# Kernel tuning notes

Measured on AMD Instinct MI355X. Metric: run time of the kernel, lower is better.

Reference implementation:

```python
import jax, jax.numpy as jnp
import numpy as np

B, C, L, OUT = 64, 256, 4096, 256
EPS = 1e-5


def setup_inputs() -> dict:
    key = jax.random.key(0)
    ks = jax.random.split(key, 8)
    s = 1.0 / np.sqrt(C)
    return {
        "x": jax.random.normal(ks[0], (B, C, L), dtype=jnp.float32),
        "Wq": jax.random.normal(ks[1], (C, C), dtype=jnp.float32) * s,
        "Wk": jax.random.normal(ks[2], (C, C), dtype=jnp.float32) * s,
        "Wv": jax.random.normal(ks[3], (C, C), dtype=jnp.float32) * s,
        "Wc": jax.random.normal(ks[4], (C, C), dtype=jnp.float32) * s,
        "Wout": jax.random.normal(ks[5], (OUT, C), dtype=jnp.float32) * s,
        "gamma": jnp.ones((C,), dtype=jnp.float32),
        "beta": jnp.zeros((C,), dtype=jnp.float32),
    }


def _conv1x1(W, x):
    # 1x1 Conv1d, no bias: (O,C) x (B,C,L) -> (B,O,L)
    return jnp.einsum("oc,bcl->bol", W, x)


def reference(x, Wq, Wk, Wv, Wc, Wout, gamma, beta):
    q = _conv1x1(Wq, x)  # (B,C,L)
    k = _conv1x1(Wk, x)  # (B,C,L)
    v = _conv1x1(Wv, x)  # (B,C,L)
    # batch-wise attention: att[b,d,l] = sum_c q[b,c,l]*k[d,c,l] / sqrt(C)
    att = jnp.einsum("bcl,dcl->bdl", q, k) / jnp.sqrt(jnp.asarray(C, x.dtype))
    att = jax.nn.softmax(att, axis=1)  # softmax over the key-batch axis
    # virt[b,c,l] = sum_d att[b,d,l] * v[d,c,l]
    virt = jnp.einsum("bdl,dcl->bcl", att, v)
    # GroupNorm(1, C): normalize over (C,L) per sample, per-channel affine
    mean = jnp.mean(virt, axis=(1, 2), keepdims=True)
    var = jnp.var(virt, axis=(1, 2), keepdims=True)
    virt = (virt - mean) * jax.lax.rsqrt(var + EPS)
    virt = virt * gamma[None, :, None] + beta[None, :, None]
    virt = jax.nn.relu(virt)
    virt = _conv1x1(Wc, virt)
    # dropout is identity in eval mode
    y = x + virt
    return _conv1x1(Wout, y)
```

## Files before the change

### kernel.cpp

```cpp
#include <hip/hip_runtime.h>


typedef __attribute__((ext_vector_type(8))) short          v8s;
typedef __attribute__((ext_vector_type(8))) unsigned short v8u;
typedef __attribute__((ext_vector_type(4))) unsigned short v4u;
typedef __attribute__((ext_vector_type(4))) float          f32x4;

#define MFMA16(a, b, c) __builtin_amdgcn_mfma_f32_16x16x32_bf16((a), (b), (c), 0, 0, 0)

static __device__ __forceinline__ unsigned short f2bf(float f) {
  union { float f; unsigned u; } v; v.f = f;
  unsigned r = (v.u + 0x7FFFu + ((v.u >> 16) & 1u)) >> 16;
  return (unsigned short)r;
}
static __device__ __forceinline__ float bf2f(unsigned short h) {
  union { unsigned u; float f; } v; v.u = ((unsigned)h) << 16; return v.f;
}

__global__ void k_prep(const float* __restrict__ Wq, const float* __restrict__ Wk,
                       const float* __restrict__ Wv, const float* __restrict__ Wc,
                       const float* __restrict__ Wout,
                       unsigned short* __restrict__ Wtv,
                       unsigned short* __restrict__ Wout2,
                       float* __restrict__ stats) {
  int bid = blockIdx.x, j = threadIdx.x;
  if (bid < 256) {
    int i = bid;
    float acc = 0.f;
    for (int c = 0; c < 256; ++c) acc += Wq[c * 256 + i] * Wk[c * 256 + j];
    Wtv[i * 256 + j] = f2bf(acc * 0.0625f);
    Wtv[(256 + i) * 256 + j] = f2bf(Wv[i * 256 + j]);
  } else if (bid < 512) {
    int o = bid - 256;
    float acc = 0.f;
    for (int c = 0; c < 256; ++c) acc += Wout[o * 256 + c] * Wc[c * 256 + j];
    Wout2[o * 512 + 256 + j] = f2bf(acc);
    Wout2[o * 512 + j] = f2bf(Wout[o * 256 + j]);
  } else {
    stats[(bid - 512) * 256 + j] = 0.f;
  }
}

__global__ void k_transpose(const float* __restrict__ x, unsigned short* __restrict__ Xt) {
  __shared__ float tile[64 * 65];
  int bid = blockIdx.x;
  int b = bid >> 8, cb = (bid >> 6) & 3, lb = bid & 63;
  int c0 = cb * 64, l0 = lb * 64, t = threadIdx.x;
#pragma unroll
  for (int i = 0; i < 4; ++i) {
    int idx = i * 256 + t, r = idx >> 4, ch = idx & 15;
    float4 v = *(const float4*)(x + ((size_t)(b * 256 + c0 + r)) * 4096 + l0 + ch * 4);
    tile[r * 65 + ch * 4 + 0] = v.x; tile[r * 65 + ch * 4 + 1] = v.y;
    tile[r * 65 + ch * 4 + 2] = v.z; tile[r * 65 + ch * 4 + 3] = v.w;
  }
  __syncthreads();
#pragma unroll
  for (int i = 0; i < 2; ++i) {
    int idx = i * 256 + t, r = idx >> 3, ch = idx & 7;
    v8u o;
#pragma unroll
    for (int j = 0; j < 8; ++j) o[j] = f2bf(tile[(ch * 8 + j) * 65 + r]);
    *(v8u*)(Xt + ((size_t)(b * 4096 + l0 + r)) * 256 + c0 + ch * 8) = o;
  }
}

__global__ __launch_bounds__(512, 4) void k_fused(const unsigned short* __restrict__ Xt,
                                                  const unsigned short* __restrict__ Wtv,
                                                  unsigned short* __restrict__ Virt,
                                                  float* __restrict__ stats) {
  extern __shared__ char smem[];
  unsigned short* Xs  = (unsigned short*)(smem);
  unsigned short* Tb  = (unsigned short*)(smem + 33792);
  unsigned short* Ps  = (unsigned short*)(smem + 70656);
  float*          red = (float*)(smem + 79872);
  float*          rowv= (float*)(smem + 80896);

  int l = blockIdx.x, t = threadIdx.x, lane = t & 63, w = t >> 6;
  int fr = lane & 15, kq = (lane >> 4) * 8, qr = (lane >> 4) * 4;

#pragma unroll
  for (int i = 0; i < 4; ++i) {
    int idx = i * 512 + t, r = idx >> 5, ch = idx & 31;
    *(v8u*)(Xs + r * 264 + ch * 8) = *(const v8u*)(Xt + ((size_t)(r * 4096 + l)) * 256 + ch * 8);
  }
  __syncthreads();

  {
    int n0 = w * 32;
    f32x4 acc[4][2];
#pragma unroll
    for (int mi = 0; mi < 4; ++mi)
#pragma unroll
      for (int nj = 0; nj < 2; ++nj) acc[mi][nj] = (f32x4){0.f, 0.f, 0.f, 0.f};
#pragma unroll
    for (int kc = 0; kc < 8; ++kc) {
      v8s a[4], b[2];
#pragma unroll
      for (int mi = 0; mi < 4; ++mi) a[mi] = *(const v8s*)(Xs + (mi * 16 + fr) * 264 + kc * 32 + kq);
#pragma unroll
      for (int nj = 0; nj < 2; ++nj)
        b[nj] = *(const v8s*)(Wtv + ((size_t)(n0 + nj * 16 + fr)) * 256 + kc * 32 + kq);
#pragma unroll
      for (int mi = 0; mi < 4; ++mi)
#pragma unroll
        for (int nj = 0; nj < 2; ++nj) acc[mi][nj] = MFMA16(a[mi], b[nj], acc[mi][nj]);
    }
#pragma unroll
    for (int mi = 0; mi < 4; ++mi)
#pragma unroll
      for (int nj = 0; nj < 2; ++nj)
#pragma unroll
        for (int i = 0; i < 4; ++i)
          Tb[(mi * 16 + qr + i) * 264 + n0 + nj * 16 + fr] = f2bf(acc[mi][nj][i]);
  }
  __syncthreads();

  int b0 = (w & 3) * 16, dp = (w >> 2) * 2, half = w >> 2;
  f32x4 sacc[2];
  sacc[0] = (f32x4){0.f, 0.f, 0.f, 0.f};
  sacc[1] = (f32x4){0.f, 0.f, 0.f, 0.f};
  {
#pragma unroll
    for (int kc = 0; kc < 8; ++kc) {
      v8s bb = *(const v8s*)(Xs + (b0 + fr) * 264 + kc * 32 + kq);
#pragma unroll
      for (int j = 0; j < 2; ++j) {
        v8s a = *(const v8s*)(Tb + ((dp + j) * 16 + fr) * 264 + kc * 32 + kq);
        sacc[j] = MFMA16(a, bb, sacc[j]);
      }
    }
    float pm = -1e30f;
#pragma unroll
    for (int j = 0; j < 2; ++j)
#pragma unroll
      for (int i = 0; i < 4; ++i) pm = fmaxf(pm, sacc[j][i]);
    pm = fmaxf(pm, __shfl_xor(pm, 16));
    pm = fmaxf(pm, __shfl_xor(pm, 32));
    if (lane < 16) red[(b0 + lane) * 4 + half] = pm;
  }
  __syncthreads();

  {
    float m = fmaxf(red[(b0 + fr) * 4 + 0], red[(b0 + fr) * 4 + 1]);
    float ps = 0.f;
#pragma unroll
    for (int j = 0; j < 2; ++j) {
      v4u pk;
#pragma unroll
      for (int i = 0; i < 4; ++i) {
        float e = __expf(sacc[j][i] - m);
        ps += e;
        pk[i] = f2bf(e);
      }
      *(v4u*)(Ps + (b0 + fr) * 72 + (dp + j) * 16 + qr) = pk;
    }
    ps += __shfl_xor(ps, 16);
    ps += __shfl_xor(ps, 32);
    if (lane < 16) red[(b0 + lane) * 4 + 2 + half] = ps;
  }

  {
    int c0 = w * 32;
    f32x4 vacc[2][4];
#pragma unroll
    for (int ci = 0; ci < 2; ++ci)
#pragma unroll
      for (int di = 0; di < 4; ++di) vacc[ci][di] = (f32x4){0.f, 0.f, 0.f, 0.f};
#pragma unroll
    for (int kc = 0; kc < 8; ++kc) {
      v8s a[2], b[4];
#pragma unroll
      for (int ci = 0; ci < 2; ++ci)
        a[ci] = *(const v8s*)(Wtv + ((size_t)(256 + c0 + ci * 16 + fr)) * 256 + kc * 32 + kq);
#pragma unroll
      for (int di = 0; di < 4; ++di) b[di] = *(const v8s*)(Xs + (di * 16 + fr) * 264 + kc * 32 + kq);
#pragma unroll
      for (int ci = 0; ci < 2; ++ci)
#pragma unroll
        for (int di = 0; di < 4; ++di) vacc[ci][di] = MFMA16(a[ci], b[di], vacc[ci][di]);
    }
#pragma unroll
    for (int ci = 0; ci < 2; ++ci)
#pragma unroll
      for (int di = 0; di < 4; ++di)
#pragma unroll
        for (int i = 0; i < 4; ++i)
          Tb[(c0 + ci * 16 + qr + i) * 72 + di * 16 + fr] = f2bf(vacc[ci][di][i]);
  }
  __syncthreads();

  if (t < 64) rowv[t] = 1.f / (red[t * 4 + 2] + red[t * 4 + 3]);

  f32x4 pacc[4][2];
#pragma unroll
  for (int mi = 0; mi < 4; ++mi) { pacc[mi][0] = (f32x4){0,0,0,0}; pacc[mi][1] = (f32x4){0,0,0,0}; }
  {
    int n0 = w * 32;
#pragma unroll
    for (int kc = 0; kc < 2; ++kc) {
      v8s a[4], b[2];
#pragma unroll
      for (int mi = 0; mi < 4; ++mi) a[mi] = *(const v8s*)(Ps + (mi * 16 + fr) * 72 + kc * 32 + kq);
#pragma unroll
      for (int nj = 0; nj < 2; ++nj)
        b[nj] = *(const v8s*)(Tb + (n0 + nj * 16 + fr) * 72 + kc * 32 + kq);
#pragma unroll
      for (int mi = 0; mi < 4; ++mi)
#pragma unroll
        for (int nj = 0; nj < 2; ++nj) pacc[mi][nj] = MFMA16(a[mi], b[nj], pacc[mi][nj]);
    }
  }
  __syncthreads();

  {
    int n0 = w * 32;
#pragma unroll
    for (int mi = 0; mi < 4; ++mi)
#pragma unroll
      for (int i = 0; i < 4; ++i) {
        float inv = rowv[mi * 16 + qr + i];
#pragma unroll
        for (int nj = 0; nj < 2; ++nj)
          Tb[(mi * 16 + qr + i) * 264 + n0 + nj * 16 + fr] = f2bf(pacc[mi][nj][i] * inv);
      }
  }
  __syncthreads();

  {
    int r = t >> 3, seg = t & 7;
    float s = 0.f, s2 = 0.f;
#pragma unroll
    for (int c4 = 0; c4 < 4; ++c4) {
      v8u v = *(const v8u*)(Tb + r * 264 + seg * 32 + c4 * 8);
#pragma unroll
      for (int j = 0; j < 8; ++j) { float f = bf2f(v[j]); s += f; s2 += f * f; }
      *(v8u*)(Virt + ((size_t)(r * 4096 + l)) * 256 + seg * 32 + c4 * 8) = v;
    }
#pragma unroll
    for (int o = 4; o > 0; o >>= 1) { s += __shfl_xor(s, o); s2 += __shfl_xor(s2, o); }
    if (seg == 0) {
      int slot = blockIdx.x & 31;
      atomicAdd(&stats[slot * 128 + r], s);
      atomicAdd(&stats[slot * 128 + 64 + r], s2);
    }
  }
}

__global__ void k_finalize(float* __restrict__ stats) {
  int t = threadIdx.x;
  if (t < 64) {
    float s = 0.f, s2 = 0.f;
    for (int sl = 0; sl < 32; ++sl) { s += stats[sl * 128 + t]; s2 += stats[sl * 128 + 64 + t]; }
    const float inv = 1.f / 1048576.f;
    float m = s * inv;
    float var = s2 * inv - m * m;
    stats[4096 + t] = m;
    stats[4160 + t] = rsqrtf(var + 1e-5f);
  }
}

__global__ void k_gemm_out(const unsigned short* __restrict__ Xt,
                           const unsigned short* __restrict__ Virt,
                           const unsigned short* __restrict__ Wout2,
                           const float* __restrict__ stats,
                           const float* __restrict__ gamma,
                           const float* __restrict__ beta,
                           float* __restrict__ out) {
  __shared__ unsigned short As[64 * 72];
  __shared__ unsigned short Bs[256 * 72];
  int t = threadIdx.x, lane = t & 63, wv = t >> 6;
  size_t t0 = (size_t)blockIdx.x * 64;
  int b = (int)(t0 >> 12);
  float mean = stats[4096 + b], rstd = stats[4160 + b];
  int n0 = wv * 64;
  f32x4 acc[4][4];
#pragma unroll
  for (int mi = 0; mi < 4; ++mi)
#pragma unroll
    for (int ni = 0; ni < 4; ++ni) acc[mi][ni] = (f32x4){0.f, 0.f, 0.f, 0.f};
  for (int kc = 0; kc < 8; ++kc) {
    __syncthreads();
#pragma unroll
    for (int i = 0; i < 2; ++i) {
      int idx = i * 256 + t, r = idx >> 3, ch = idx & 7;
      if (kc < 4) {
        *(v8u*)(As + r * 72 + ch * 8) = *(const v8u*)(Xt + (t0 + r) * 256 + kc * 64 + ch * 8);
      } else {
        v8u v = *(const v8u*)(Virt + (t0 + r) * 256 + (kc - 4) * 64 + ch * 8);
        int cb = (kc - 4) * 64 + ch * 8;
        float4 g0 = *(const float4*)(gamma + cb), g1 = *(const float4*)(gamma + cb + 4);
        float4 bb0 = *(const float4*)(beta + cb), bb1 = *(const float4*)(beta + cb + 4);
        float gs[8] = {g0.x, g0.y, g0.z, g0.w, g1.x, g1.y, g1.z, g1.w};
        float bs[8] = {bb0.x, bb0.y, bb0.z, bb0.w, bb1.x, bb1.y, bb1.z, bb1.w};
        v8u o;
#pragma unroll
        for (int j = 0; j < 8; ++j) {
          float z = (bf2f(v[j]) - mean) * rstd * gs[j] + bs[j];
          o[j] = f2bf(fmaxf(z, 0.f));
        }
        *(v8u*)(As + r * 72 + ch * 8) = o;
      }
    }
#pragma unroll
    for (int i = 0; i < 8; ++i) {
      int idx = i * 256 + t, r = idx >> 3, ch = idx & 7;
      *(v8u*)(Bs + r * 72 + ch * 8) = *(const v8u*)(Wout2 + r * 512 + kc * 64 + ch * 8);
    }
    __syncthreads();
#pragma unroll
    for (int ks = 0; ks < 2; ++ks) {
      int kq = ks * 32 + (lane >> 4) * 8;
      v8s a[4], bb[4];
#pragma unroll
      for (int mi = 0; mi < 4; ++mi) a[mi] = *(const v8s*)(As + (mi * 16 + (lane & 15)) * 72 + kq);
#pragma unroll
      for (int ni = 0; ni < 4; ++ni)
        bb[ni] = *(const v8s*)(Bs + (n0 + ni * 16 + (lane & 15)) * 72 + kq);
#pragma unroll
      for (int mi = 0; mi < 4; ++mi)
#pragma unroll
        for (int ni = 0; ni < 4; ++ni) acc[mi][ni] = MFMA16(a[mi], bb[ni], acc[mi][ni]);
    }
  }
  int qr = (lane >> 4) * 4, lbase = (int)(t0 & 4095);
#pragma unroll
  for (int mi = 0; mi < 4; ++mi)
#pragma unroll
    for (int ni = 0; ni < 4; ++ni)
#pragma unroll
      for (int i = 0; i < 4; ++i) {
        int ll = lbase + mi * 16 + qr + i;
        int o = n0 + ni * 16 + (lane & 15);
        out[((size_t)(b * 256 + o)) * 4096 + ll] = acc[mi][ni][i];
      }
}

extern "C" void kernel_launch(void* const* d_in, const int* in_sizes, int n_in,
                              void* d_out, int out_size, void* d_ws, size_t ws_size,
                              hipStream_t stream) {
  const float* x     = (const float*)d_in[0];
  const float* Wq    = (const float*)d_in[1];
  const float* Wk    = (const float*)d_in[2];
  const float* Wv    = (const float*)d_in[3];
  const float* Wc    = (const float*)d_in[4];
  const float* Wout  = (const float*)d_in[5];
  const float* gamma = (const float*)d_in[6];
  const float* beta  = (const float*)d_in[7];
  float* out = (float*)d_out;
  char* ws = (char*)d_ws;
  unsigned short* Xt   = (unsigned short*)(ws);
  unsigned short* Virt = (unsigned short*)(ws + 134217728ull);
  unsigned short* Wtv  = (unsigned short*)(ws + 268435456ull);
  unsigned short* W2   = (unsigned short*)(ws + 268697600ull);
  float* stats         = (float*)(ws + 268959744ull);

  static const int kFusedLds = 81152;
  hipFuncSetAttribute((const void*)k_fused, hipFuncAttributeMaxDynamicSharedMemorySize,
                      kFusedLds);

  k_prep<<<528, 256, 0, stream>>>(Wq, Wk, Wv, Wc, Wout, Wtv, W2, stats);
  k_transpose<<<16384, 256, 0, stream>>>(x, Xt);
  k_fused<<<4096, 512, kFusedLds, stream>>>(Xt, Wtv, Virt, stats);
  k_finalize<<<1, 64, 0, stream>>>(stats);
  k_gemm_out<<<4096, 256, 0, stream>>>(Xt, Virt, W2, stats, gamma, beta, out);
}
```

Measured before the change: 863.8 us.

## Restructure output GEMM with larger tiles, async global-to-LDS double buffering, swizzle

The output GEMM now uses 256-row tiles with 512 threads arranged as 2x4 waves, so each 256-column weight tile staged in LDS is reused across four times as many rows. Tiles are loaded straight into LDS through global_load_lds with an XOR swizzle and double-buffered, so the next K-chunk loads while the current one runs MFMAs. The GroupNorm, affine and ReLU step on Virt is applied in place in LDS after the async load, with folded scale/shift constants. In exchange it uses 128KB of LDS per block (likely one block per CU despite launch_bounds(512,2)), adds an extra barrier on normalization steps, and uses a much larger accumulator set per thread.

```diff
diff --git a/kernel.cpp b/kernel.cpp
--- a/kernel.cpp
+++ b/kernel.cpp
@@ -7,6 +7,11 @@
 typedef __attribute__((ext_vector_type(4))) float          f32x4;
 
 #define MFMA16(a, b, c) __builtin_amdgcn_mfma_f32_16x16x32_bf16((a), (b), (c), 0, 0, 0)
+
+#define GLOAD16(g, l)                                                            \
+  __builtin_amdgcn_global_load_lds(                                              \
+      (const __attribute__((address_space(1))) unsigned int*)(const void*)(g),   \
+      (__attribute__((address_space(3))) unsigned int*)(void*)(l), 16, 0, 0)
 
 static __device__ __forceinline__ unsigned short f2bf(float f) {
   union { float f; unsigned u; } v; v.f = f;
@@ -259,78 +264,117 @@
   }
 }
 
-__global__ void k_gemm_out(const unsigned short* __restrict__ Xt,
-                           const unsigned short* __restrict__ Virt,
-                           const unsigned short* __restrict__ Wout2,
-                           const float* __restrict__ stats,
-                           const float* __restrict__ gamma,
-                           const float* __restrict__ beta,
-                           float* __restrict__ out) {
-  __shared__ unsigned short As[64 * 72];
-  __shared__ unsigned short Bs[256 * 72];
-  int t = threadIdx.x, lane = t & 63, wv = t >> 6;
-  size_t t0 = (size_t)blockIdx.x * 64;
+__global__ __launch_bounds__(512, 2) void k_gemm_out(const unsigned short* __restrict__ Xt,
+                                                     const unsigned short* __restrict__ Virt,
+                                                     const unsigned short* __restrict__ Wout2,
+                                                     const float* __restrict__ stats,
+                                                     const float* __restrict__ gamma,
+                                                     const float* __restrict__ beta,
+                                                     float* __restrict__ out) {
+  extern __shared__ char smem[];
+  int t = threadIdx.x, lane = t & 63, w = t >> 6;
+  int fr = lane & 15;
+  int wm = w >> 2, wn = w & 3;
+  size_t t0 = (size_t)blockIdx.x * 256;
   int b = (int)(t0 >> 12);
   float mean = stats[4096 + b], rstd = stats[4160 + b];
-  int n0 = wv * 64;
-  f32x4 acc[4][4];
-#pragma unroll
-  for (int mi = 0; mi < 4; ++mi)
+
+  f32x4 acc[8][4];
+#pragma unroll
+  for (int mi = 0; mi < 8; ++mi)
 #pragma unroll
     for (int ni = 0; ni < 4; ++ni) acc[mi][ni] = (f32x4){0.f, 0.f, 0.f, 0.f};
+
+  int srow = (lane >> 3);
+  int sph = lane & 7;
+
+#define STAGE_TILE(BUF, KC)                                                          \
+  do {                                                                               \
+    char* base_ = smem + (BUF) * 65536;                                              \
+    if (w < 4) {                                                                     \
+      const unsigned short* s0_ =                                                    \
+          ((KC) < 4) ? (Xt + (KC) * 64) : (Virt + ((KC) - 4) * 64);                  \
+      _Pragma("unroll") for (int g_ = 0; g_ < 8; ++g_) {                             \
+        int r_ = w * 64 + g_ * 8 + srow;                                             \
+        int sl_ = sph ^ (r_ & 7);                                                    \
+        GLOAD16(s0_ + (t0 + r_) * 256 + sl_ * 8, base_ + w * 8192 + g_ * 1024);      \
+      }                                                                              \
+    } else {                                                                         \
+      int wb_ = w - 4;                                                               \
+      _Pragma("unroll") for (int g_ = 0; g_ < 8; ++g_) {                             \
+        int r_ = wb_ * 64 + g_ * 8 + srow;                                           \
+        int sl_ = sph ^ (r_ & 7);                                                    \
+        GLOAD16(Wout2 + r_ * 512 + (KC) * 64 + sl_ * 8,                              \
+                base_ + 32768 + wb_ * 8192 + g_ * 1024);                             \
+      }                                                                              \
+    }                                                                                \
+  } while (0)
+
+  STAGE_TILE(0, 0);
+  __syncthreads();
+
   for (int kc = 0; kc < 8; ++kc) {
+    int cur = kc & 1;
+    if (kc < 7) STAGE_TILE(cur ^ 1, kc + 1);
+
+    {
+      const char* Ab = smem + cur * 65536;
+      const char* Bb = Ab + 32768;
+#pragma unroll
+      for (int ks = 0; ks < 2; ++ks) {
+        int xr = (ks * 64 + (lane >> 4) * 16) ^ ((fr & 7) << 4);
+        v8s a[8], bb[4];
+#pragma unroll
+        for (int mi = 0; mi < 8; ++mi)
+          a[mi] = *(const v8s*)(Ab + (wm * 128 + mi * 16 + fr) * 128 + xr);
+#pragma unroll
+        for (int ni = 0; ni < 4; ++ni)
+          bb[ni] = *(const v8s*)(Bb + (wn * 64 + ni * 16 + fr) * 128 + xr);
+#pragma unroll
+        for (int mi = 0; mi < 8; ++mi)
+#pragma unroll
+          for (int ni = 0; ni < 4; ++ni) acc[mi][ni] = MFMA16(a[mi], bb[ni], acc[mi][ni]);
+      }
+    }
     __syncthreads();
-#pragma unroll
-    for (int i = 0; i < 2; ++i) {
-      int idx = i * 256 + t, r = idx >> 3, ch = idx & 7;
-      if (kc < 4) {
-        *(v8u*)(As + r * 72 + ch * 8) = *(const v8u*)(Xt + (t0 + r) * 256 + kc * 64 + ch * 8);
-      } else {
-        v8u v = *(const v8u*)(Virt + (t0 + r) * 256 + (kc - 4) * 64 + ch * 8);
-        int cb = (kc - 4) * 64 + ch * 8;
-        float4 g0 = *(const float4*)(gamma + cb), g1 = *(const float4*)(gamma + cb + 4);
-        float4 bb0 = *(const float4*)(beta + cb), bb1 = *(const float4*)(beta + cb + 4);
-        float gs[8] = {g0.x, g0.y, g0.z, g0.w, g1.x, g1.y, g1.z, g1.w};
-        float bs[8] = {bb0.x, bb0.y, bb0.z, bb0.w, bb1.x, bb1.y, bb1.z, bb1.w};
-        v8u o;
-#pragma unroll
-        for (int j = 0; j < 8; ++j) {
-          float z = (bf2f(v[j]) - mean) * rstd * gs[j] + bs[j];
-          o[j] = f2bf(fmaxf(z, 0.f));
+
+    if (kc < 7 && kc >= 3) {
+      char* Ab = smem + (cur ^ 1) * 65536;
+      int s_log = sph ^ ((t >> 3) & 7);
+      int cb = (kc + 1 - 4) * 64 + s_log * 8;
+      float4 g0 = *(const float4*)(gamma + cb), g1 = *(const float4*)(gamma + cb + 4);
+      float4 b0 = *(const float4*)(beta + cb), b1 = *(const float4*)(beta + cb + 4);
+      float rg[8] = {g0.x * rstd, g0.y * rstd, g0.z * rstd, g0.w * rstd,
+                     g1.x * rstd, g1.y * rstd, g1.z * rstd, g1.w * rstd};
+      float sh[8] = {b0.x - mean * rg[0], b0.y - mean * rg[1], b0.z - mean * rg[2],
+                     b0.w - mean * rg[3], b1.x - mean * rg[4], b1.y - mean * rg[5],
+                     b1.z - mean * rg[6], b1.w - mean * rg[7]};
+#pragma unroll
+      for (int j = 0; j < 4; ++j) {
+        int r = j * 64 + (t >> 3);
+        v8u* p = (v8u*)(Ab + r * 128 + sph * 16);
+        v8u v = *p, o;
+#pragma unroll
+        for (int e = 0; e < 8; ++e) {
+          float z = fmaf(bf2f(v[e]), rg[e], sh[e]);
+          o[e] = f2bf(fmaxf(z, 0.f));
         }
-        *(v8u*)(As + r * 72 + ch * 8) = o;
-      }
-    }
-#pragma unroll
-    for (int i = 0; i < 8; ++i) {
-      int idx = i * 256 + t, r = idx >> 3, ch = idx & 7;
-      *(v8u*)(Bs + r * 72 + ch * 8) = *(const v8u*)(Wout2 + r * 512 + kc * 64 + ch * 8);
-    }
-    __syncthreads();
-#pragma unroll
-    for (int ks = 0; ks < 2; ++ks) {
-      int kq = ks * 32 + (lane >> 4) * 8;
-      v8s a[4], bb[4];
-#pragma unroll
-      for (int mi = 0; mi < 4; ++mi) a[mi] = *(const v8s*)(As + (mi * 16 + (lane & 15)) * 72 + kq);
-#pragma unroll
-      for (int ni = 0; ni < 4; ++ni)
-        bb[ni] = *(const v8s*)(Bs + (n0 + ni * 16 + (lane & 15)) * 72 + kq);
-#pragma unroll
-      for (int mi = 0; mi < 4; ++mi)
-#pragma unroll
-        for (int ni = 0; ni < 4; ++ni) acc[mi][ni] = MFMA16(a[mi], bb[ni], acc[mi][ni]);
-    }
-  }
+        *p = o;
+      }
+      __syncthreads();
+    }
+  }
+#undef STAGE_TILE
+
   int qr = (lane >> 4) * 4, lbase = (int)(t0 & 4095);
 #pragma unroll
-  for (int mi = 0; mi < 4; ++mi)
+  for (int mi = 0; mi < 8; ++mi)
 #pragma unroll
     for (int ni = 0; ni < 4; ++ni)
 #pragma unroll
       for (int i = 0; i < 4; ++i) {
-        int ll = lbase + mi * 16 + qr + i;
-        int o = n0 + ni * 16 + (lane & 15);
+        int ll = lbase + wm * 128 + mi * 16 + qr + i;
+        int o = wn * 64 + ni * 16 + fr;
         out[((size_t)(b * 256 + o)) * 4096 + ll] = acc[mi][ni][i];
       }
 }
@@ -355,12 +399,15 @@
   float* stats         = (float*)(ws + 268959744ull);
 
   static const int kFusedLds = 81152;
+  static const int kGemmLds  = 131072;
   hipFuncSetAttribute((const void*)k_fused, hipFuncAttributeMaxDynamicSharedMemorySize,
                       kFusedLds);
+  hipFuncSetAttribute((const void*)k_gemm_out, hipFuncAttributeMaxDynamicSharedMemorySize,
+                      kGemmLds);
 
   k_prep<<<528, 256, 0, stream>>>(Wq, Wk, Wv, Wc, Wout, Wtv, W2, stats);
   k_transpose<<<16384, 256, 0, stream>>>(x, Xt);
   k_fused<<<4096, 512, kFusedLds, stream>>>(Xt, Wtv, Virt, stats);
   k_finalize<<<1, 64, 0, stream>>>(stats);
-  k_gemm_out<<<4096, 256, 0, stream>>>(Xt, Virt, W2, stats, gamma, beta, out);
-}
+  k_gemm_out<<<1024, 512, kGemmLds, stream>>>(Xt, Virt, W2, stats, gamma, beta, out);
+}
```

New measurement: 797.9 us. 1.08x faster.
